# Performance work log

Measured on AMD Instinct MI355X. Metric: run time of the kernel, lower is better.

The kernel has to match this reference:

```python
import jax, jax.numpy as jnp
import numpy as np

N_SRC = 50000
N_DST = 50000
IN_FEATS = 256
OUT_FEATS = 32
NUM_HEADS = 4
N_EDGES = 800000


def setup_inputs() -> dict:
    key = jax.random.key(0)
    ks = jax.random.split(key, 7)
    h_src = jax.random.normal(ks[0], (N_SRC, IN_FEATS), dtype=jnp.float32)
    h_dst = jax.random.normal(ks[1], (N_DST, IN_FEATS), dtype=jnp.float32)
    # xavier-normal-ish scaling for the shared fc weight
    W = jax.random.normal(ks[2], (IN_FEATS, NUM_HEADS * OUT_FEATS), dtype=jnp.float32) * (
        jnp.sqrt(2.0) * jnp.sqrt(2.0 / (IN_FEATS + NUM_HEADS * OUT_FEATS))
    )
    attn_l = jax.random.normal(ks[3], (NUM_HEADS, OUT_FEATS), dtype=jnp.float32) * 0.1
    attn_r = jax.random.normal(ks[4], (NUM_HEADS, OUT_FEATS), dtype=jnp.float32) * 0.1
    src_idx = jax.random.randint(ks[5], (N_EDGES,), 0, N_SRC, dtype=jnp.int32)
    dst_idx = jax.random.randint(ks[6], (N_EDGES,), 0, N_DST, dtype=jnp.int32)
    return {"h_src": h_src, "h_dst": h_dst, "W": W, "attn_l": attn_l,
            "attn_r": attn_r, "src_idx": src_idx, "dst_idx": dst_idx}


def reference(h_src, h_dst, W, attn_l, attn_r, src_idx, dst_idx):
    H, F = NUM_HEADS, OUT_FEATS
    # shared linear projection (no bias), reshape to [N, H, F]
    ft_src = (h_src @ W).reshape(-1, H, F)            # [N_src, H, F]
    ft_dst = (h_dst @ W).reshape(-1, H, F)            # [N_dst, H, F]
    # per-node attention logits, [N, H]
    el = jnp.einsum('nhf,hf->nh', ft_src, attn_l)
    er = jnp.einsum('nhf,hf->nh', ft_dst, attn_r)
    # u_add_v gather over edges, LeakyReLU(0.2) -> [E, H]
    e = jax.nn.leaky_relu(el[src_idx] + er[dst_idx], negative_slope=0.2)
    # edge softmax over incoming edges of each destination node
    smax = jax.ops.segment_max(e, dst_idx, num_segments=N_DST)   # [N_dst, H]
    e_exp = jnp.exp(e - smax[dst_idx])                           # [E, H]
    ssum = jax.ops.segment_sum(e_exp, dst_idx, num_segments=N_DST)
    a = e_exp / ssum[dst_idx]                                    # [E, H]
    # u_mul_e + scatter-sum aggregation -> [N_dst, H, F]
    msg = ft_src[src_idx] * a[:, :, None]
    rst = jax.ops.segment_sum(msg, dst_idx, num_segments=N_DST)
    return rst
```

## Files before the change

kernel.cpp:

```cpp
#include <hip/hip_runtime.h>

#define IN_FEATS 256
#define OUT_FEATS 32
#define NUM_HEADS 4
#define NHF 128

typedef __attribute__((ext_vector_type(8))) short short8;
typedef __attribute__((ext_vector_type(4))) float f32x4;

__device__ inline unsigned short f2bf(float f) {
    unsigned int u = __builtin_bit_cast(unsigned int, f);
    u = (u + 0x7fff + ((u >> 16) & 1)) >> 16;
    return (unsigned short)u;
}
__device__ inline float bfhi2f(unsigned int packed_hi) {
    return __builtin_bit_cast(float, packed_hi);
}

__global__ __launch_bounds__(256) void prep(const float* __restrict__ W,
                                            const float* __restrict__ attn_r,
                                            float* __restrict__ v,
                                            unsigned short* __restrict__ Wt) {
    if (blockIdx.x < 128) {
        int n = blockIdx.x;
        int k = threadIdx.x;
        Wt[n * 256 + k] = f2bf(W[(size_t)k * NHF + n]);
    } else {
        for (int p = threadIdx.x; p < IN_FEATS * NUM_HEADS; p += 256) {
            int k = p >> 2, h = p & 3;
            const float* wr = W + (size_t)k * NHF + h * OUT_FEATS;
            const float* ar = attn_r + h * OUT_FEATS;
            float s = 0.f;
            #pragma unroll
            for (int f = 0; f < OUT_FEATS; ++f) s += wr[f] * ar[f];
            v[p] = s;
        }
    }
}

__global__ __launch_bounds__(256) void gemm_el(const float* __restrict__ A,
                                               const unsigned short* __restrict__ Wt,
                                               const float* __restrict__ attn_l,
                                               unsigned short* __restrict__ ft16,
                                               float* __restrict__ el, int M) {
    __shared__ unsigned short WtL[128 * 256];

    const int wave = threadIdx.x >> 6;
    const int lane = threadIdx.x & 63;
    const int quad = lane >> 4;
    const int mc   = lane & 15;
    const int row_base = blockIdx.x * 64 + wave * 16;

    for (int i = threadIdx.x; i < 4096; i += 256) {
        const int n = i >> 5, c = i & 31;
        const int cs = (c + n) & 31;
        *(uint4*)(WtL + n * 256 + cs * 8) = *(const uint4*)(Wt + n * 256 + c * 8);
    }

    float al[8];
    #pragma unroll
    for (int t = 0; t < 8; ++t) al[t] = attn_l[(t >> 1) * 32 + (t & 1) * 16 + mc];

    const int rowA = min(row_base + mc, M - 1);
    const float* arow = A + (size_t)rowA * IN_FEATS;

    float4 a[8][2];
    #pragma unroll
    for (int kk = 0; kk < 8; ++kk) {
        a[kk][0] = *(const float4*)(arow + kk * 32 + quad * 8);
        a[kk][1] = *(const float4*)(arow + kk * 32 + quad * 8 + 4);
    }

    f32x4 acc[8];
    #pragma unroll
    for (int t = 0; t < 8; ++t) acc[t] = (f32x4){0.f, 0.f, 0.f, 0.f};

    __syncthreads();

    #pragma unroll
    for (int kk = 0; kk < 8; ++kk) {
        short8 af;
        af[0] = (short)f2bf(a[kk][0].x); af[1] = (short)f2bf(a[kk][0].y);
        af[2] = (short)f2bf(a[kk][0].z); af[3] = (short)f2bf(a[kk][0].w);
        af[4] = (short)f2bf(a[kk][1].x); af[5] = (short)f2bf(a[kk][1].y);
        af[6] = (short)f2bf(a[kk][1].z); af[7] = (short)f2bf(a[kk][1].w);
        #pragma unroll
        for (int t = 0; t < 8; ++t) {
            const int n = t * 16 + mc;
            const int c = ((kk << 2) + quad + n) & 31;
            const short8 bf = *(const short8*)(WtL + n * 256 + c * 8);
            acc[t] = __builtin_amdgcn_mfma_f32_16x16x32_bf16(af, bf, acc[t], 0, 0, 0);
        }
    }

    float elp[4][4];
    #pragma unroll
    for (int v = 0; v < 4; ++v)
        #pragma unroll
        for (int h = 0; h < 4; ++h) elp[v][h] = 0.f;
    #pragma unroll
    for (int v = 0; v < 4; ++v)
        #pragma unroll
        for (int t = 0; t < 8; ++t) elp[v][t >> 1] += acc[t][v] * al[t];
    #pragma unroll
    for (int v = 0; v < 4; ++v)
        #pragma unroll
        for (int h = 0; h < 4; ++h) {
            #pragma unroll
            for (int d = 1; d < 16; d <<= 1)
                elp[v][h] += __shfl_xor(elp[v][h], d, 64);
        }

    #pragma unroll
    for (int v = 0; v < 4; ++v) {
        const int rg = row_base + quad * 4 + v;
        if (rg < M) {
            unsigned short* o = ft16 + (size_t)rg * NHF;
            #pragma unroll
            for (int t = 0; t < 8; ++t) o[t * 16 + mc] = f2bf(acc[t][v]);
            if (mc < 4) {
                float ev = (mc == 0) ? elp[v][0] : (mc == 1) ? elp[v][1]
                         : (mc == 2) ? elp[v][2] : elp[v][3];
                el[(size_t)rg * 4 + mc] = ev;
            }
        }
    }
}

__global__ __launch_bounds__(256) void compute_er(const float* __restrict__ hdst,
                                                  const float* __restrict__ v,
                                                  float* __restrict__ er, int M) {
    int wid  = (blockIdx.x * blockDim.x + threadIdx.x) >> 6;
    int lane = threadIdx.x & 63;
    if (wid >= M) return;
    const float4 x = *(const float4*)(hdst + (size_t)wid * IN_FEATS + lane * 4);
    const float4* vp = (const float4*)(v + (size_t)lane * 16);
    float4 v0 = vp[0], v1 = vp[1], v2 = vp[2], v3 = vp[3];
    float a0 = x.x * v0.x + x.y * v1.x + x.z * v2.x + x.w * v3.x;
    float a1 = x.x * v0.y + x.y * v1.y + x.z * v2.y + x.w * v3.y;
    float a2 = x.x * v0.z + x.y * v1.z + x.z * v2.z + x.w * v3.z;
    float a3 = x.x * v0.w + x.y * v1.w + x.z * v2.w + x.w * v3.w;
    #pragma unroll
    for (int m = 32; m >= 1; m >>= 1) {
        a0 += __shfl_xor(a0, m, 64);
        a1 += __shfl_xor(a1, m, 64);
        a2 += __shfl_xor(a2, m, 64);
        a3 += __shfl_xor(a3, m, 64);
    }
    if (lane == 0) *(float4*)(er + (size_t)wid * 4) = make_float4(a0, a1, a2, a3);
}


__global__ __launch_bounds__(256) void bucket_hist(const int* __restrict__ dst,
                                                   int* __restrict__ bcnt, int E) {
    __shared__ int h[256];
    h[threadIdx.x] = 0;
    __syncthreads();
    for (int e = blockIdx.x * 256 + threadIdx.x; e < E; e += gridDim.x * 256)
        atomicAdd(&h[dst[e] >> 8], 1);
    __syncthreads();
    int c = h[threadIdx.x];
    if (c) atomicAdd(&bcnt[threadIdx.x], c);
}

__global__ __launch_bounds__(256) void bucket_scan(const int* __restrict__ bcnt,
                                                   int* __restrict__ bbase,
                                                   int* __restrict__ bcursor,
                                                   int* __restrict__ off, int n_dst, int E) {
    __shared__ int s[256];
    int t = threadIdx.x;
    int v = bcnt[t];
    s[t] = v;
    __syncthreads();
    #pragma unroll
    for (int d = 1; d < 256; d <<= 1) {
        int x = (t >= d) ? s[t - d] : 0;
        __syncthreads();
        s[t] += x;
        __syncthreads();
    }
    int ex = s[t] - v;
    bbase[t] = ex;
    bcursor[t] = ex;
    if (t == 255) bbase[256] = s[255];
    if (t == 0) off[n_dst] = E;
}

__global__ __launch_bounds__(256) void bin_pairs(const int* __restrict__ src,
                                                 const int* __restrict__ dst,
                                                 int* __restrict__ bcursor,
                                                 int2* __restrict__ pairs, int E) {
    __shared__ int cnt[256];
    __shared__ int basel[256];
    const int e0 = blockIdx.x * 4096;
    const int e1 = min(e0 + 4096, E);
    const int t = threadIdx.x;
    cnt[t] = 0;
    __syncthreads();
    for (int e = e0 + t; e < e1; e += 256)
        atomicAdd(&cnt[dst[e] >> 8], 1);
    __syncthreads();
    int c = cnt[t];
    basel[t] = c ? atomicAdd(&bcursor[t], c) : 0;
    __syncthreads();
    cnt[t] = 0;
    __syncthreads();
    for (int e = e0 + t; e < e1; e += 256) {
        int d = dst[e];
        int b = d >> 8;
        int o = atomicAdd(&cnt[b], 1);
        pairs[basel[b] + o] = make_int2(src[e], d);
    }
}

__global__ __launch_bounds__(256) void fine_csr(const int2* __restrict__ pairs,
                                                const int* __restrict__ bbase,
                                                int* __restrict__ off,
                                                int* __restrict__ csr_src, int n_dst) {
    __shared__ int cnt[256];
    __shared__ int cur[256];
    const int b = blockIdx.x;
    const int p0 = bbase[b], p1 = bbase[b + 1];
    const int t = threadIdx.x;
    cnt[t] = 0;
    __syncthreads();
    for (int p = p0 + t; p < p1; p += 256)
        atomicAdd(&cnt[pairs[p].y & 255], 1);
    __syncthreads();
    int v = cnt[t];
    cur[t] = v;
    __syncthreads();
    #pragma unroll
    for (int d = 1; d < 256; d <<= 1) {
        int x = (t >= d) ? cur[t - d] : 0;
        __syncthreads();
        cur[t] += x;
        __syncthreads();
    }
    int ex = cur[t] - v;
    int node = b * 256 + t;
    if (node < n_dst) off[node] = p0 + ex;
    __syncthreads();
    cur[t] = ex;
    __syncthreads();
    for (int p = p0 + t; p < p1; p += 256) {
        int2 pr = pairs[p];
        int o = atomicAdd(&cur[pr.y & 255], 1);
        csr_src[p0 + o] = pr.x;
    }
}

__global__ __launch_bounds__(256) void agg_pull(const int* __restrict__ off,
                                                const int* __restrict__ csr_src,
                                                const float* __restrict__ el,
                                                const float* __restrict__ er,
                                                const uint2* __restrict__ ftp,
                                                float* __restrict__ out, int n_dst) {
    const int wid  = (blockIdx.x * blockDim.x + threadIdx.x) >> 6;
    const int lane = threadIdx.x & 63;
    const int half = lane >> 5;
    const int hl   = lane & 31;
    const int node = wid * 2 + half;
    const bool valid = node < n_dst;
    const int nc = valid ? node : 0;
    const int h  = hl >> 3;
    const float er_h = er[nc * 4 + h];
    const int start = off[nc];
    const int end   = valid ? off[nc + 1] : start;
    const int deg   = end - start;
    const int last  = max(end - 1, 0);

    const int sl = csr_src[min(start + hl, last)];

    const int mdeg  = max(deg, __shfl_xor(deg, 32, 64));
    const int iters = (min(mdeg, 32) + 3) >> 2;

    float a0 = 0.f, a1 = 0.f, a2 = 0.f, a3 = 0.f, sw = 0.f;

    int s0 = __shfl(sl, 0, 32), s1 = __shfl(sl, 1, 32),
        s2 = __shfl(sl, 2, 32), s3 = __shfl(sl, 3, 32);
    float e0 = el[s0 * 4 + h], e1 = el[s1 * 4 + h],
          e2 = el[s2 * 4 + h], e3 = el[s3 * 4 + h];
    uint2 q0 = ftp[s0 * 32 + hl], q1 = ftp[s1 * 32 + hl],
          q2 = ftp[s2 * 32 + hl], q3 = ftp[s3 * 32 + hl];

    for (int i = 0; i < iters; ++i) {
        const int jn = (i + 1) << 2;
        const int t0 = __shfl(sl, min(jn,     31), 32);
        const int t1 = __shfl(sl, min(jn + 1, 31), 32);
        const int t2 = __shfl(sl, min(jn + 2, 31), 32);
        const int t3 = __shfl(sl, min(jn + 3, 31), 32);
        const float f0 = el[t0 * 4 + h], f1 = el[t1 * 4 + h],
                    f2 = el[t2 * 4 + h], f3 = el[t3 * 4 + h];
        const uint2 r0 = ftp[t0 * 32 + hl], r1 = ftp[t1 * 32 + hl],
                    r2 = ftp[t2 * 32 + hl], r3 = ftp[t3 * 32 + hl];

        const int kb = start + (i << 2);
        float x0 = e0 + er_h, x1 = e1 + er_h, x2 = e2 + er_h, x3 = e3 + er_h;
        x0 = fmaxf(x0, 0.2f * x0);
        x1 = fmaxf(x1, 0.2f * x1);
        x2 = fmaxf(x2, 0.2f * x2);
        x3 = fmaxf(x3, 0.2f * x3);
        const float w0 = (kb     < end) ? __expf(x0) : 0.f;
        const float w1 = (kb + 1 < end) ? __expf(x1) : 0.f;
        const float w2 = (kb + 2 < end) ? __expf(x2) : 0.f;
        const float w3 = (kb + 3 < end) ? __expf(x3) : 0.f;
        sw += (w0 + w1) + (w2 + w3);
        a0 = fmaf(bfhi2f(q0.x << 16),          w0, a0);
        a1 = fmaf(bfhi2f(q0.x & 0xffff0000u),  w0, a1);
        a2 = fmaf(bfhi2f(q0.y << 16),          w0, a2);
        a3 = fmaf(bfhi2f(q0.y & 0xffff0000u),  w0, a3);
        a0 = fmaf(bfhi2f(q1.x << 16),          w1, a0);
        a1 = fmaf(bfhi2f(q1.x & 0xffff0000u),  w1, a1);
        a2 = fmaf(bfhi2f(q1.y << 16),          w1, a2);
        a3 = fmaf(bfhi2f(q1.y & 0xffff0000u),  w1, a3);
        a0 = fmaf(bfhi2f(q2.x << 16),          w2, a0);
        a1 = fmaf(bfhi2f(q2.x & 0xffff0000u),  w2, a1);
        a2 = fmaf(bfhi2f(q2.y << 16),          w2, a2);
        a3 = fmaf(bfhi2f(q2.y & 0xffff0000u),  w2, a3);
        a0 = fmaf(bfhi2f(q3.x << 16),          w3, a0);
        a1 = fmaf(bfhi2f(q3.x & 0xffff0000u),  w3, a1);
        a2 = fmaf(bfhi2f(q3.y << 16),          w3, a2);
        a3 = fmaf(bfhi2f(q3.y & 0xffff0000u),  w3, a3);

        e0 = f0; e1 = f1; e2 = f2; e3 = f3;
        q0 = r0; q1 = r1; q2 = r2; q3 = r3;
    }

    for (int k = start + 32; k < end; ++k) {
        const int s = csr_src[k];
        float x = el[s * 4 + h] + er_h;
        x = fmaxf(x, 0.2f * x);
        const float w = __expf(x);
        const uint2 q = ftp[s * 32 + hl];
        sw += w;
        a0 = fmaf(bfhi2f(q.x << 16),         w, a0);
        a1 = fmaf(bfhi2f(q.x & 0xffff0000u), w, a1);
        a2 = fmaf(bfhi2f(q.y << 16),         w, a2);
        a3 = fmaf(bfhi2f(q.y & 0xffff0000u), w, a3);
    }

    if (valid) {
        const float inv = (deg > 0) ? 1.f / sw : 0.f;
        float4 r;
        r.x = a0 * inv; r.y = a1 * inv; r.z = a2 * inv; r.w = a3 * inv;
        *(float4*)(out + (size_t)node * NHF + hl * 4) = r;
    }
}

extern "C" void kernel_launch(void* const* d_in, const int* in_sizes, int n_in,
                              void* d_out, int out_size, void* d_ws, size_t ws_size,
                              hipStream_t stream) {
    const float* h_src  = (const float*)d_in[0];
    const float* h_dst  = (const float*)d_in[1];
    const float* W      = (const float*)d_in[2];
    const float* attn_l = (const float*)d_in[3];
    const float* attn_r = (const float*)d_in[4];
    const int* src_idx  = (const int*)d_in[5];
    const int* dst_idx  = (const int*)d_in[6];

    const int n_src = in_sizes[0] / IN_FEATS;
    const int n_dst = in_sizes[1] / IN_FEATS;
    const int E     = in_sizes[5];

    const int nbuck = (n_dst + 255) >> 8;

    char* ws = (char*)d_ws;
    size_t o = 0;
    float* v       = (float*)(ws + o); o += 4096;
    float* el      = (float*)(ws + o); o += (size_t)n_src * 4 * sizeof(float);
    float* er      = (float*)(ws + o); o += (size_t)n_dst * 4 * sizeof(float);
    int*   off     = (int*)(ws + o);   o += ((size_t)n_dst + 16) * sizeof(int);
    int*   bcnt    = (int*)(ws + o);   o += 256 * sizeof(int);
    int*   bbase   = (int*)(ws + o);   o += 260 * sizeof(int);
    int*   bcursor = (int*)(ws + o);   o += 256 * sizeof(int);
    unsigned short* Wt = (unsigned short*)(ws + o); o += (size_t)NHF * IN_FEATS * sizeof(unsigned short);
    int*   csr_src = (int*)(ws + o);   o += (size_t)E * sizeof(int);
    int2*  pairs   = (int2*)(ws + o);  o += (size_t)E * sizeof(int2);
    unsigned short* ft16 = (unsigned short*)(ws + o); o += (size_t)n_src * NHF * sizeof(unsigned short);

    float* out = (float*)d_out;

    (void)hipMemsetAsync(bcnt, 0, 256 * sizeof(int), stream);

    prep<<<129, 256, 0, stream>>>(W, attn_r, v, Wt);
    gemm_el<<<(n_src + 63) / 64, 256, 0, stream>>>(h_src, Wt, attn_l, ft16, el, n_src);
    compute_er<<<(n_dst + 3) / 4, 256, 0, stream>>>(h_dst, v, er, n_dst);
    bucket_hist<<<512, 256, 0, stream>>>(dst_idx, bcnt, E);
    bucket_scan<<<1, 256, 0, stream>>>(bcnt, bbase, bcursor, off, n_dst, E);
    bin_pairs<<<(E + 4095) / 4096, 256, 0, stream>>>(src_idx, dst_idx, bcursor, pairs, E);
    fine_csr<<<nbuck, 256, 0, stream>>>(pairs, bbase, off, csr_src, n_dst);
    {
        const int nwave = (n_dst + 1) >> 1;
        agg_pull<<<(nwave + 3) / 4, 256, 0, stream>>>(off, csr_src, el, er,
                                                      (const uint2*)ft16, out, n_dst);
    }
}
```

Before: 258.2 us.

## Pack CSR pairs, stage ft16 stores via LDS, deepen gather prefetch, drop memset

Several independent changes. The bf16 projection output is staged through shared memory so each row is written with coalesced 16-byte stores instead of scattered 2-byte stores. The (src,dst) pairs are packed into one 32-bit word (16-bit src plus 8-bit local dst), which halves pair traffic but assumes source indices fit in 16 bits, and N_SRC=50000 does. The aggregation loop now prefetches 8 neighbors instead of 4, and the bucket-count memset is folded into the prep kernel to remove one launch.

New measurement: 255.0 us. About the same (-1.2%).

```diff
diff --git a/kernel.cpp b/kernel.cpp
--- a/kernel.cpp
+++ b/kernel.cpp
@@ -20,12 +20,14 @@
 __global__ __launch_bounds__(256) void prep(const float* __restrict__ W,
                                             const float* __restrict__ attn_r,
                                             float* __restrict__ v,
-                                            unsigned short* __restrict__ Wt) {
+                                            unsigned short* __restrict__ Wt,
+                                            int* __restrict__ bcnt) {
     if (blockIdx.x < 128) {
         int n = blockIdx.x;
         int k = threadIdx.x;
         Wt[n * 256 + k] = f2bf(W[(size_t)k * NHF + n]);
     } else {
+        bcnt[threadIdx.x] = 0;
         for (int p = threadIdx.x; p < IN_FEATS * NUM_HEADS; p += 256) {
             int k = p >> 2, h = p & 3;
             const float* wr = W + (size_t)k * NHF + h * OUT_FEATS;
@@ -38,6 +40,7 @@
     }
 }
 
+#define BSTRIDE 136
 __global__ __launch_bounds__(256) void gemm_el(const float* __restrict__ A,
                                                const unsigned short* __restrict__ Wt,
                                                const float* __restrict__ attn_l,
@@ -114,16 +117,28 @@
     #pragma unroll
     for (int v = 0; v < 4; ++v) {
         const int rg = row_base + quad * 4 + v;
-        if (rg < M) {
-            unsigned short* o = ft16 + (size_t)rg * NHF;
-            #pragma unroll
-            for (int t = 0; t < 8; ++t) o[t * 16 + mc] = f2bf(acc[t][v]);
-            if (mc < 4) {
-                float ev = (mc == 0) ? elp[v][0] : (mc == 1) ? elp[v][1]
-                         : (mc == 2) ? elp[v][2] : elp[v][3];
-                el[(size_t)rg * 4 + mc] = ev;
-            }
-        }
+        if (rg < M && mc < 4) {
+            float ev = (mc == 0) ? elp[v][0] : (mc == 1) ? elp[v][1]
+                     : (mc == 2) ? elp[v][2] : elp[v][3];
+            el[(size_t)rg * 4 + mc] = ev;
+        }
+    }
+
+    __syncthreads();
+    #pragma unroll
+    for (int v = 0; v < 4; ++v) {
+        const int lr = wave * 16 + quad * 4 + v;
+        #pragma unroll
+        for (int t = 0; t < 8; ++t)
+            WtL[lr * BSTRIDE + t * 16 + mc] = f2bf(acc[t][v]);
+    }
+    __syncthreads();
+    const int rows_in_blk = min(64, M - blockIdx.x * 64);
+    for (int i = threadIdx.x; i < 64 * 16; i += 256) {
+        const int lr = i >> 4, seg = i & 15;
+        if (lr < rows_in_blk)
+            *(uint4*)(ft16 + (size_t)(blockIdx.x * 64 + lr) * NHF + seg * 8) =
+                *(const uint4*)(WtL + lr * BSTRIDE + seg * 8);
     }
 }
 
@@ -189,7 +204,7 @@
 __global__ __launch_bounds__(256) void bin_pairs(const int* __restrict__ src,
                                                  const int* __restrict__ dst,
                                                  int* __restrict__ bcursor,
-                                                 int2* __restrict__ pairs, int E) {
+                                                 unsigned int* __restrict__ pairs, int E) {
     __shared__ int cnt[256];
     __shared__ int basel[256];
     const int e0 = blockIdx.x * 4096;
@@ -209,11 +224,11 @@
         int d = dst[e];
         int b = d >> 8;
         int o = atomicAdd(&cnt[b], 1);
-        pairs[basel[b] + o] = make_int2(src[e], d);
-    }
-}
-
-__global__ __launch_bounds__(256) void fine_csr(const int2* __restrict__ pairs,
+        pairs[basel[b] + o] = (unsigned int)src[e] | ((unsigned int)(d & 255) << 16);
+    }
+}
+
+__global__ __launch_bounds__(256) void fine_csr(const unsigned int* __restrict__ pairs,
                                                 const int* __restrict__ bbase,
                                                 int* __restrict__ off,
                                                 int* __restrict__ csr_src, int n_dst) {
@@ -225,7 +240,7 @@
     cnt[t] = 0;
     __syncthreads();
     for (int p = p0 + t; p < p1; p += 256)
-        atomicAdd(&cnt[pairs[p].y & 255], 1);
+        atomicAdd(&cnt[pairs[p] >> 16], 1);
     __syncthreads();
     int v = cnt[t];
     cur[t] = v;
@@ -244,9 +259,9 @@
     cur[t] = ex;
     __syncthreads();
     for (int p = p0 + t; p < p1; p += 256) {
-        int2 pr = pairs[p];
-        int o = atomicAdd(&cur[pr.y & 255], 1);
-        csr_src[p0 + o] = pr.x;
+        unsigned int pr = pairs[p];
+        int o = atomicAdd(&cur[pr >> 16], 1);
+        csr_src[p0 + o] = (int)(pr & 0xffffu);
     }
 }
 
@@ -273,58 +288,43 @@
     const int sl = csr_src[min(start + hl, last)];
 
     const int mdeg  = max(deg, __shfl_xor(deg, 32, 64));
-    const int iters = (min(mdeg, 32) + 3) >> 2;
+    const int iters = (min(mdeg, 32) + 7) >> 3;
 
     float a0 = 0.f, a1 = 0.f, a2 = 0.f, a3 = 0.f, sw = 0.f;
 
-    int s0 = __shfl(sl, 0, 32), s1 = __shfl(sl, 1, 32),
-        s2 = __shfl(sl, 2, 32), s3 = __shfl(sl, 3, 32);
-    float e0 = el[s0 * 4 + h], e1 = el[s1 * 4 + h],
-          e2 = el[s2 * 4 + h], e3 = el[s3 * 4 + h];
-    uint2 q0 = ftp[s0 * 32 + hl], q1 = ftp[s1 * 32 + hl],
-          q2 = ftp[s2 * 32 + hl], q3 = ftp[s3 * 32 + hl];
+    float e[8]; uint2 q[8];
+    #pragma unroll
+    for (int j = 0; j < 8; ++j) {
+        const int s = __shfl(sl, j, 32);
+        e[j] = el[s * 4 + h];
+        q[j] = ftp[s * 32 + hl];
+    }
 
     for (int i = 0; i < iters; ++i) {
-        const int jn = (i + 1) << 2;
-        const int t0 = __shfl(sl, min(jn,     31), 32);
-        const int t1 = __shfl(sl, min(jn + 1, 31), 32);
-        const int t2 = __shfl(sl, min(jn + 2, 31), 32);
-        const int t3 = __shfl(sl, min(jn + 3, 31), 32);
-        const float f0 = el[t0 * 4 + h], f1 = el[t1 * 4 + h],
-                    f2 = el[t2 * 4 + h], f3 = el[t3 * 4 + h];
-        const uint2 r0 = ftp[t0 * 32 + hl], r1 = ftp[t1 * 32 + hl],
-                    r2 = ftp[t2 * 32 + hl], r3 = ftp[t3 * 32 + hl];
-
-        const int kb = start + (i << 2);
-        float x0 = e0 + er_h, x1 = e1 + er_h, x2 = e2 + er_h, x3 = e3 + er_h;
-        x0 = fmaxf(x0, 0.2f * x0);
-        x1 = fmaxf(x1, 0.2f * x1);
-        x2 = fmaxf(x2, 0.2f * x2);
-        x3 = fmaxf(x3, 0.2f * x3);
-        const float w0 = (kb     < end) ? __expf(x0) : 0.f;
-        const float w1 = (kb + 1 < end) ? __expf(x1) : 0.f;
-        const float w2 = (kb + 2 < end) ? __expf(x2) : 0.f;
-        const float w3 = (kb + 3 < end) ? __expf(x3) : 0.f;
-        sw += (w0 + w1) + (w2 + w3);
-        a0 = fmaf(bfhi2f(q0.x << 16),          w0, a0);
-        a1 = fmaf(bfhi2f(q0.x & 0xffff0000u),  w0, a1);
-        a2 = fmaf(bfhi2f(q0.y << 16),          w0, a2);
-        a3 = fmaf(bfhi2f(q0.y & 0xffff0000u),  w0, a3);
-        a0 = fmaf(bfhi2f(q1.x << 16),          w1, a0);
-        a1 = fmaf(bfhi2f(q1.x & 0xffff0000u),  w1, a1);
-        a2 = fmaf(bfhi2f(q1.y << 16),          w1, a2);
-        a3 = fmaf(bfhi2f(q1.y & 0xffff0000u),  w1, a3);
-        a0 = fmaf(bfhi2f(q2.x << 16),          w2, a0);
-        a1 = fmaf(bfhi2f(q2.x & 0xffff0000u),  w2, a1);
-        a2 = fmaf(bfhi2f(q2.y << 16),          w2, a2);
-        a3 = fmaf(bfhi2f(q2.y & 0xffff0000u),  w2, a3);
-        a0 = fmaf(bfhi2f(q3.x << 16),          w3, a0);
-        a1 = fmaf(bfhi2f(q3.x & 0xffff0000u),  w3, a1);
-        a2 = fmaf(bfhi2f(q3.y << 16),          w3, a2);
-        a3 = fmaf(bfhi2f(q3.y & 0xffff0000u),  w3, a3);
-
-        e0 = f0; e1 = f1; e2 = f2; e3 = f3;
-        q0 = r0; q1 = r1; q2 = r2; q3 = r3;
+        float f[8]; uint2 r[8];
+        const int jn = (i + 1) << 3;
+        #pragma unroll
+        for (int j = 0; j < 8; ++j) {
+            const int s = __shfl(sl, min(jn + j, 31), 32);
+            f[j] = el[s * 4 + h];
+            r[j] = ftp[s * 32 + hl];
+        }
+
+        const int kb = start + (i << 3);
+        #pragma unroll
+        for (int j = 0; j < 8; ++j) {
+            float x = e[j] + er_h;
+            x = fmaxf(x, 0.2f * x);
+            const float w = (kb + j < end) ? __expf(x) : 0.f;
+            sw += w;
+            a0 = fmaf(bfhi2f(q[j].x << 16),          w, a0);
+            a1 = fmaf(bfhi2f(q[j].x & 0xffff0000u),  w, a1);
+            a2 = fmaf(bfhi2f(q[j].y << 16),          w, a2);
+            a3 = fmaf(bfhi2f(q[j].y & 0xffff0000u),  w, a3);
+        }
+
+        #pragma unroll
+        for (int j = 0; j < 8; ++j) { e[j] = f[j]; q[j] = r[j]; }
     }
 
     for (int k = start + 32; k < end; ++k) {
@@ -332,12 +332,12 @@
         float x = el[s * 4 + h] + er_h;
         x = fmaxf(x, 0.2f * x);
         const float w = __expf(x);
-        const uint2 q = ftp[s * 32 + hl];
+        const uint2 qq = ftp[s * 32 + hl];
         sw += w;
-        a0 = fmaf(bfhi2f(q.x << 16),         w, a0);
-        a1 = fmaf(bfhi2f(q.x & 0xffff0000u), w, a1);
-        a2 = fmaf(bfhi2f(q.y << 16),         w, a2);
-        a3 = fmaf(bfhi2f(q.y & 0xffff0000u), w, a3);
+        a0 = fmaf(bfhi2f(qq.x << 16),         w, a0);
+        a1 = fmaf(bfhi2f(qq.x & 0xffff0000u), w, a1);
+        a2 = fmaf(bfhi2f(qq.y << 16),         w, a2);
+        a3 = fmaf(bfhi2f(qq.y & 0xffff0000u), w, a3);
     }
 
     if (valid) {
@@ -376,14 +376,12 @@
     int*   bcursor = (int*)(ws + o);   o += 256 * sizeof(int);
     unsigned short* Wt = (unsigned short*)(ws + o); o += (size_t)NHF * IN_FEATS * sizeof(unsigned short);
     int*   csr_src = (int*)(ws + o);   o += (size_t)E * sizeof(int);
-    int2*  pairs   = (int2*)(ws + o);  o += (size_t)E * sizeof(int2);
+    unsigned int* pairs = (unsigned int*)(ws + o); o += (size_t)E * sizeof(unsigned int);
     unsigned short* ft16 = (unsigned short*)(ws + o); o += (size_t)n_src * NHF * sizeof(unsigned short);
 
     float* out = (float*)d_out;
 
-    (void)hipMemsetAsync(bcnt, 0, 256 * sizeof(int), stream);
-
-    prep<<<129, 256, 0, stream>>>(W, attn_r, v, Wt);
+    prep<<<129, 256, 0, stream>>>(W, attn_r, v, Wt, bcnt);
     gemm_el<<<(n_src + 63) / 64, 256, 0, stream>>>(h_src, Wt, attn_l, ft16, el, n_src);
     compute_er<<<(n_dst + 3) / 4, 256, 0, stream>>>(h_dst, v, er, n_dst);
     bucket_hist<<<512, 256, 0, stream>>>(dst_idx, bcnt, E);
```
